# Kernel optimization log

Hardware: AMD Instinct MI355X
Metric: run time of the kernel (lower is better)

Reference implementation:

```python
import jax, jax.numpy as jnp
import numpy as np

NUM_CLASSES = 5
DIM = 512
NUM_HEADS = 8
B, N = 8, 256


def setup_inputs() -> dict:
    key = jax.random.key(0)
    ks = jax.random.split(key, 7)
    s = 1.0 / np.sqrt(DIM)
    return {
        "x": jax.random.normal(ks[0], (B, N, DIM), dtype=jnp.float32),
        "anchors": jax.random.normal(ks[1], (NUM_CLASSES, N, DIM), dtype=jnp.float32),
        "weights": jax.random.uniform(ks[2], (B, NUM_HEADS, NUM_CLASSES), dtype=jnp.float32),
        "qk_w": jax.random.normal(ks[3], (DIM, DIM), dtype=jnp.float32) * s,
        "v_w": jax.random.normal(ks[4], (DIM, DIM), dtype=jnp.float32) * s,
        "proj_w": jax.random.normal(ks[5], (DIM, DIM), dtype=jnp.float32) * s,
        "proj_b": jnp.zeros((DIM,), dtype=jnp.float32),
    }


def reference(x, anchors, weights, qk_w, v_w, proj_w, proj_b):
    Bx, Nx, C = x.shape
    H = NUM_HEADS
    hd = C // H
    scale = hd ** (-0.5)

    # v: [B, H, N, hd]
    v = (x @ v_w.T).reshape(Bx, Nx, H, hd).transpose(0, 2, 1, 3)
    # q: [B, H, N, hd]; k: [cls, H, N, hd] (shared qk projection)
    q = (x @ qk_w.T).reshape(Bx, Nx, H, hd).transpose(0, 2, 1, 3)
    k = (anchors @ qk_w.T).reshape(NUM_CLASSES, Nx, H, hd).transpose(0, 2, 1, 3)

    # a0: [B, cls, H, N, N]
    a0 = jnp.einsum("bhnd,chmd->bchnm", q, k) * scale
    left = jax.nn.relu(-a0)                         # relu of negative branch
    right = jax.nn.relu(jnp.swapaxes(a0, -2, -1))   # relu of transposed positive branch
    # second large NxN matmul, then softmax over dim=-2 (columns)
    attn = jax.nn.softmax(left @ right, axis=-2)    # [B, cls, H, N, N]

    # class-weighted combine: weights [B, H, cls] -> tmp [B, H, N, N]
    tmp = jnp.einsum("bhc,bchnm->bhnm", weights, attn)

    # (tmp @ v): [B, H, N, hd]; torch reshapes directly to (B, N, C) without permute
    out = (tmp @ v).reshape(Bx, Nx, C)
    out = out @ proj_w.T + proj_b
    return (out, a0)
```

## Files before the change

kernel.cpp:

```cpp
#include <hip/hip_runtime.h>
#include <hip/hip_fp16.h>
#include <cstdint>

#define BB 8
#define NN 256
#define NC 5
#define NH 8
#define DIM 512
#define HD 64

typedef _Float16 half_t;
typedef _Float16 h8 __attribute__((ext_vector_type(8)));
typedef _Float16 h4 __attribute__((ext_vector_type(4)));
typedef float f4 __attribute__((ext_vector_type(4)));
typedef uint32_t u4v __attribute__((ext_vector_type(4)));

__device__ __forceinline__ f4 mfma16(h8 a, h8 b, f4 c) {
  return __builtin_amdgcn_mfma_f32_16x16x32_f16(a, b, c, 0, 0, 0);
}

static __device__ const h8 HZERO = {(_Float16)0, (_Float16)0, (_Float16)0, (_Float16)0,
                                    (_Float16)0, (_Float16)0, (_Float16)0, (_Float16)0};

__device__ __forceinline__ h8 relu_pos_h8(h8 x) {
#if __has_builtin(__builtin_elementwise_max)
  return __builtin_elementwise_max(x, HZERO);
#else
  u4v u = __builtin_bit_cast(u4v, x);
  const u4v k1 = {0x00010001u, 0x00010001u, 0x00010001u, 0x00010001u};
  u4v s = (u >> 15) & k1;
  u4v m = (s << 16) - s;
  u = u & ~m;
  return __builtin_bit_cast(h8, u);
#endif
}

__device__ __forceinline__ h8 relu_neg_h8(h8 x) {
#if __has_builtin(__builtin_elementwise_max)
  return __builtin_elementwise_max(-x, HZERO);
#else
  u4v u = __builtin_bit_cast(u4v, x);
  const u4v k1 = {0x00010001u, 0x00010001u, 0x00010001u, 0x00010001u};
  const u4v ks = {0x80008000u, 0x80008000u, 0x80008000u, 0x80008000u};
  u4v s = (u >> 15) & k1;
  u4v m = (s << 16) - s;
  u = (u ^ ks) & m;
  return __builtin_bit_cast(h8, u);
#endif
}

__device__ __forceinline__ void barrier_lds() {
  __builtin_amdgcn_sched_barrier(0);
  asm volatile("s_waitcnt lgkmcnt(0)" ::: "memory");
  __builtin_amdgcn_s_barrier();
  asm volatile("" ::: "memory");
  __builtin_amdgcn_sched_barrier(0);
}

__global__ __launch_bounds__(256) void cvt_all(const float* __restrict__ x,
                                               const float* __restrict__ anchors,
                                               const float* __restrict__ qk_w,
                                               const float* __restrict__ v_w,
                                               const float* __restrict__ proj_w,
                                               half_t* __restrict__ x_h,
                                               half_t* __restrict__ anc_h,
                                               half_t* __restrict__ qk_h,
                                               half_t* __restrict__ v_wh,
                                               half_t* __restrict__ pw_h) {
  int i = blockIdx.x * 256 + threadIdx.x;
  const float* src;
  half_t* dst;
  int off;
  if (i < 262144)      { src = x;       dst = x_h;   off = i; }
  else if (i < 425984) { src = anchors; dst = anc_h; off = i - 262144; }
  else if (i < 491520) { src = qk_w;    dst = qk_h;  off = i - 425984; }
  else if (i < 557056) { src = v_w;     dst = v_wh;  off = i - 491520; }
  else                 { src = proj_w;  dst = pw_h;  off = i - 557056; }
  float4 v = ((const float4*)src)[off];
  h4 o;
  o[0] = (_Float16)v.x; o[1] = (_Float16)v.y; o[2] = (_Float16)v.z; o[3] = (_Float16)v.w;
  ((h4*)dst)[off] = o;
}

__global__ __launch_bounds__(256) void proj_all(const half_t* __restrict__ x_h,
                                                const half_t* __restrict__ anc_h,
                                                const half_t* __restrict__ qk_h,
                                                const half_t* __restrict__ v_wh,
                                                half_t* __restrict__ q_h,
                                                half_t* __restrict__ k_h,
                                                half_t* __restrict__ vT) {
  const int bx = blockIdx.x, by = blockIdx.y;
  const int tid = threadIdx.x;
  const int w = tid >> 6, lane = tid & 63;
  const int lr = lane & 15, lk = (lane >> 4) * 8, lg = lane >> 4;

  const half_t* A;
  const half_t* W;
  int mode, rt0;
  if (bx < 32)      { A = x_h;   W = qk_h; mode = 0; rt0 = bx * 64; }
  else if (bx < 52) { A = anc_h; W = qk_h; mode = 1; rt0 = (bx - 32) * 64; }
  else              { A = x_h;   W = v_wh; mode = 2; rt0 = (bx - 52) * 64; }

  const int row0 = rt0 + w * 16;
  const int col0 = by * 64;
  const f4 fz = {0.f, 0.f, 0.f, 0.f};
  f4 acc[4] = {fz, fz, fz, fz};
  const half_t* arow = A + (size_t)(row0 + lr) * DIM;

  if (mode != 2) {
    for (int k0 = 0; k0 < DIM; k0 += 32) {
      h8 a = *(const h8*)(arow + k0 + lk);
#pragma unroll
      for (int ct = 0; ct < 4; ++ct) {
        h8 b = *(const h8*)(W + (size_t)(col0 + ct * 16 + lr) * DIM + k0 + lk);
        acc[ct] = mfma16(a, b, acc[ct]);
      }
    }
    half_t* out = (mode == 0) ? q_h : k_h;
#pragma unroll
    for (int ct = 0; ct < 4; ++ct) {
      int col = col0 + ct * 16 + lr;
#pragma unroll
      for (int r = 0; r < 4; ++r) {
        int row = row0 + lg * 4 + r;
        out[(size_t)row * DIM + col] = (half_t)acc[ct][r];
      }
    }
  } else {
    for (int k0 = 0; k0 < DIM; k0 += 32) {
      h8 a = *(const h8*)(arow + k0 + lk);
#pragma unroll
      for (int ct = 0; ct < 4; ++ct) {
        h8 b = *(const h8*)(W + (size_t)(col0 + ct * 16 + lr) * DIM + k0 + lk);
        acc[ct] = mfma16(b, a, acc[ct]);
      }
    }
    const int xrow = row0 + lr;
#pragma unroll
    for (int ct = 0; ct < 4; ++ct) {
#pragma unroll
      for (int r = 0; r < 4; ++r) {
        int col = col0 + ct * 16 + lg * 4 + r;
        vT[(size_t)col * (BB * NN) + xrow] = (half_t)acc[ct][r];
      }
    }
  }
}

__global__ __launch_bounds__(1024, 4) void fused_attn8(const half_t* __restrict__ q_h,
                                                       const half_t* __restrict__ k_h,
                                                       const half_t* __restrict__ vT,
                                                       const float* __restrict__ weights,
                                                       float* __restrict__ a0_base,
                                                       half_t* __restrict__ U4) {
  extern __shared__ char smem[];
  half_t* a0s = (half_t*)smem;
  half_t* kst = (half_t*)(smem + 98304);
  half_t* vst = (half_t*)smem;
  half_t* pbuf = (half_t*)(smem + 32768);
  float2* scr = (float2*)(smem + 131072);
  float2* scr2 = (float2*)(smem + 147456);

  const int id = blockIdx.x;
  const int b = id / 40;
  const int rem = id % 40;
  const int c = rem / 8;
  const int h = rem & 7;

  const int tid = threadIdx.x;
  const int w = tid >> 6, lane = tid & 63;
  const int lr = lane & 15, lk = (lane >> 4) * 8, lg = lane >> 4;
  const int n0 = w * 16;
  const int sg = w & 7, cg = w >> 3;

  const half_t* qb = q_h + (size_t)(b * NN) * DIM + h * HD;
  const half_t* kb = k_h + (size_t)(c * NN) * DIM + h * HD;
  const half_t* vTb = vT + (size_t)(h * HD) * (BB * NN) + b * NN;
  float* a0out = a0_base + (size_t)((b * NC + c) * NH + h) * (NN * NN);
  const float wgt = weights[(b * NH + h) * NC + c];

  const f4 fz = {0.f, 0.f, 0.f, 0.f};

  h8 qf0 = *(const h8*)(qb + (size_t)(n0 + lr) * DIM + lk);
  h8 qf1 = *(const h8*)(qb + (size_t)(n0 + lr) * DIM + 32 + lk);

#pragma unroll
  for (int pass = 0; pass < 2; ++pass) {
    int slot = pass * 1024 + tid;
    int row = slot >> 3, k8 = (slot & 7) * 8;
    h8 val = *(const h8*)(kb + (size_t)row * DIM + k8);
    *(h8*)(kst + ((row * 64 + k8) ^ ((row & 7) << 3))) = val;
  }
  barrier_lds();

  f4 acc[16];
#pragma unroll
  for (int mt = 0; mt < 16; ++mt) {
    const int krow = mt * 16 + lr;
    h8 kf0 = *(const h8*)(kst + ((krow * 64 + lk) ^ ((krow & 7) << 3)));
    h8 kf1 = *(const h8*)(kst + ((krow * 64 + 32 + lk) ^ ((krow & 7) << 3)));
    acc[mt] = mfma16(kf0, qf0, fz);
    acc[mt] = mfma16(kf1, qf1, acc[mt]);
#pragma unroll
    for (int r = 0; r < 4; ++r) acc[mt][r] *= 0.125f;
  }
  barrier_lds();

  const int na = n0 + lr;
#pragma unroll
  for (int mt = 0; mt < 16; ++mt) {
    const int mb = mt * 16 + lg * 4;
    h4 hv;
#pragma unroll
    for (int r = 0; r < 4; ++r) hv[r] = (_Float16)acc[mt][r];
    *(h4*)(a0s + ((na * NN + mb) ^ ((na & 7) << 3))) = hv;
    *(f4*)(a0out + (size_t)na * NN + mb) = acc[mt];
  }
  barrier_lds();

  f4 sacc[8][2];
#pragma unroll
  for (int ct = 0; ct < 8; ++ct) {
    sacc[ct][0] = fz;
    sacc[ct][1] = fz;
  }
#pragma unroll
  for (int kc = 0; kc < 8; ++kc) {
    const int rl0 = sg * 32 + lr, rl1 = sg * 32 + 16 + lr;
    h8 La0 = relu_neg_h8(*(const h8*)(a0s + ((rl0 * NN + kc * 32 + lk) ^ ((rl0 & 7) << 3))));
    h8 La1 = relu_neg_h8(*(const h8*)(a0s + ((rl1 * NN + kc * 32 + lk) ^ ((rl1 & 7) << 3))));
#pragma unroll
    for (int ct = 0; ct < 8; ++ct) {
      const int rr = cg * 128 + ct * 16 + lr;
      h8 R = relu_pos_h8(*(const h8*)(a0s + ((rr * NN + kc * 32 + lk) ^ ((rr & 7) << 3))));
      sacc[ct][0] = mfma16(La0, R, sacc[ct][0]);
      sacc[ct][1] = mfma16(La1, R, sacc[ct][1]);
    }
  }

  float mw[8];
#pragma unroll
  for (int ct = 0; ct < 8; ++ct) {
    float v = 0.f;
#pragma unroll
    for (int rt = 0; rt < 2; ++rt)
#pragma unroll
      for (int r = 0; r < 4; ++r) v = fmaxf(v, sacc[ct][rt][r]);
    v = fmaxf(v, __shfl_xor(v, 16, 64));
    v = fmaxf(v, __shfl_xor(v, 32, 64));
    mw[ct] = v;
    float s = 0.f;
#pragma unroll
    for (int rt = 0; rt < 2; ++rt)
#pragma unroll
      for (int r = 0; r < 4; ++r) {
        float e = __expf(sacc[ct][rt][r] - v);
        sacc[ct][rt][r] = e;
        s += e;
      }
    s += __shfl_xor(s, 16, 64);
    s += __shfl_xor(s, 32, 64);
    if (lane < 16) {
      float2 t;
      t.x = v;
      t.y = s;
      scr[sg * 256 + cg * 128 + ct * 16 + lr] = t;
    }
  }
  barrier_lds();

  if (tid < 256) {
    float gm = 0.f;
#pragma unroll
    for (int ww = 0; ww < 8; ++ww) gm = fmaxf(gm, scr[ww * 256 + tid].x);
    float sg2 = 0.f;
#pragma unroll
    for (int ww = 0; ww < 8; ++ww) {
      float2 t = scr[ww * 256 + tid];
      sg2 += t.y * __expf(t.x - gm);
    }
    float2 r;
    r.x = gm;
    r.y = sg2;
    scr2[tid] = r;
  }
#pragma unroll
  for (int pass = 0; pass < 2; ++pass) {
    int slot = pass * 1024 + tid;
    int d = slot >> 5, m8 = (slot & 31) * 8;
    h8 vv = *(const h8*)(vTb + (size_t)d * (BB * NN) + m8);
    *(h8*)(vst + ((d * NN + m8) ^ ((d & 7) << 3))) = vv;
  }
  barrier_lds();

#pragma unroll
  for (int ct = 0; ct < 8; ++ct) {
    float2 t = scr2[cg * 128 + ct * 16 + lr];
    float fac = __expf(mw[ct] - t.x) * wgt / t.y;
#pragma unroll
    for (int rt = 0; rt < 2; ++rt)
#pragma unroll
      for (int r = 0; r < 4; ++r) sacc[ct][rt][r] *= fac;
  }

  half_t* pbw = pbuf + w * 1344;
  f4 uacc[4][2];
#pragma unroll
  for (int dt = 0; dt < 4; ++dt) {
    uacc[dt][0] = fz;
    uacc[dt][1] = fz;
  }
#pragma unroll
  for (int p = 0; p < 4; ++p) {
#pragma unroll
    for (int ctl = 0; ctl < 2; ++ctl) {
      const int ct = p * 2 + ctl;
#pragma unroll
      for (int rt = 0; rt < 2; ++rt) {
        h4 hv;
#pragma unroll
        for (int r = 0; r < 4; ++r) hv[r] = (_Float16)sacc[ct][rt][r];
        *(h4*)(pbw + (ctl * 16 + lr) * 42 + rt * 16 + lg * 4) = hv;
      }
    }
    h8 pf0, pf1;
#pragma unroll
    for (int e = 0; e < 8; ++e) {
      pf0[e] = pbw[(lg * 8 + e) * 42 + lr];
      pf1[e] = pbw[(lg * 8 + e) * 42 + 16 + lr];
    }
#pragma unroll
    for (int dt = 0; dt < 4; ++dt) {
      const int dr = dt * 16 + lr;
      h8 vf = *(const h8*)(vst + ((dr * NN + cg * 128 + p * 32 + lg * 8) ^ ((dr & 7) << 3)));
      uacc[dt][0] = mfma16(vf, pf0, uacc[dt][0]);
      uacc[dt][1] = mfma16(vf, pf1, uacc[dt][1]);
    }
  }

  half_t* U4b = U4 + (size_t)(((b * NC + c) * NH + h) * 2 + cg) * (NN * HD);
#pragma unroll
  for (int dt = 0; dt < 4; ++dt)
#pragma unroll
    for (int nt = 0; nt < 2; ++nt) {
      int n = sg * 32 + nt * 16 + lr;
      h4 hv;
#pragma unroll
      for (int r = 0; r < 4; ++r) hv[r] = (_Float16)uacc[dt][nt][r];
      *(h4*)(U4b + (size_t)n * HD + dt * 16 + lg * 4) = hv;
    }
}

__global__ __launch_bounds__(256) void reduce_u(const half_t* __restrict__ U4,
                                                half_t* __restrict__ out_head) {
  int t = blockIdx.x * 256 + threadIdx.x;
  int bh = t >> 11;
  int e = (t & 2047) * 8;
  int b = bh >> 3, h = bh & 7;
  float acc[8] = {0.f, 0.f, 0.f, 0.f, 0.f, 0.f, 0.f, 0.f};
#pragma unroll
  for (int c = 0; c < NC; ++c)
#pragma unroll
    for (int qq = 0; qq < 2; ++qq) {
      h8 u = *(const h8*)(U4 + (size_t)(((b * NC + c) * NH + h) * 2 + qq) * (NN * HD) + e);
#pragma unroll
      for (int j = 0; j < 8; ++j) acc[j] += (float)u[j];
    }
  h8 o;
#pragma unroll
  for (int j = 0; j < 8; ++j) o[j] = (_Float16)acc[j];
  *(h8*)(out_head + (size_t)bh * (NN * HD) + e) = o;
}

__global__ __launch_bounds__(256) void out_proj(const half_t* __restrict__ out_head,
                                                const half_t* __restrict__ pw_h,
                                                const float* __restrict__ pb,
                                                float* __restrict__ out0) {
  const int tid = threadIdx.x;
  const int w = tid >> 6, lane = tid & 63;
  const int lr = lane & 15, lk = (lane >> 4) * 8, lg = lane >> 4;
  const int row0 = blockIdx.x * 64 + w * 16;
  const int col0 = blockIdx.y * 64;
  const int r_ = row0 + lr;
  const int b = r_ >> 8, i = r_ & 255;
  const int hh = i >> 5;
  const f4 fz = {0.f, 0.f, 0.f, 0.f};
  f4 acc[4] = {fz, fz, fz, fz};
  for (int k0 = 0; k0 < DIM; k0 += 32) {
    const int k = k0 + lk;
    const int n = ((i & 31) << 3) | (k >> 6);
    const int d = k & 63;
    h8 a = *(const h8*)(out_head + (size_t)((b * NH + hh) * NN + n) * HD + d);
#pragma unroll
    for (int ct = 0; ct < 4; ++ct) {
      h8 bf = *(const h8*)(pw_h + (size_t)(col0 + ct * 16 + lr) * DIM + k0 + lk);
      acc[ct] = mfma16(a, bf, acc[ct]);
    }
  }
#pragma unroll
  for (int ct = 0; ct < 4; ++ct) {
    int col = col0 + ct * 16 + lr;
    float bias = pb[col];
#pragma unroll
    for (int r = 0; r < 4; ++r) {
      int row = row0 + lg * 4 + r;
      out0[(size_t)row * DIM + col] = acc[ct][r] + bias;
    }
  }
}

extern "C" void kernel_launch(void* const* d_in, const int* in_sizes, int n_in,
                              void* d_out, int out_size, void* d_ws, size_t ws_size,
                              hipStream_t stream) {
  const float* x = (const float*)d_in[0];
  const float* anchors = (const float*)d_in[1];
  const float* weights = (const float*)d_in[2];
  const float* qk_w = (const float*)d_in[3];
  const float* v_w = (const float*)d_in[4];
  const float* proj_w = (const float*)d_in[5];
  const float* proj_b = (const float*)d_in[6];

  float* out0 = (float*)d_out;
  float* a0_out = out0 + (size_t)BB * NN * DIM;

  char* ws = (char*)d_ws;
  const size_t MB = 1024 * 1024;
  half_t* x_h   = (half_t*)(ws);
  half_t* anc_h = (half_t*)(ws + 2 * MB);
  half_t* qk_h  = (half_t*)(ws + 3407872);
  half_t* v_wh  = (half_t*)(ws + 3932160);
  half_t* U4    = (half_t*)(ws);
  half_t* pw_h     = (half_t*)(ws + 20 * MB);
  half_t* q_h      = (half_t*)(ws + 20 * MB + 524288);
  half_t* k_h      = (half_t*)(ws + 22 * MB + 524288);
  half_t* vT       = (half_t*)(ws + 24 * MB);
  half_t* out_head = (half_t*)(ws + 26 * MB);

  cvt_all<<<dim3(2432), 256, 0, stream>>>(x, anchors, qk_w, v_w, proj_w,
                                          x_h, anc_h, qk_h, v_wh, pw_h);

  proj_all<<<dim3(84, 8), 256, 0, stream>>>(x_h, anc_h, qk_h, v_wh, q_h, k_h, vT);

  const size_t lds_bytes = 131072 + 16384 + 2048;
  fused_attn8<<<dim3(BB * NC * NH), 1024, lds_bytes, stream>>>(q_h, k_h, vT, weights,
                                                               a0_out, U4);

  reduce_u<<<dim3(512), 256, 0, stream>>>(U4, out_head);

  out_proj<<<dim3(32, 8), 256, 0, stream>>>(out_head, pw_h, proj_b, out0);

  (void)in_sizes; (void)n_in; (void)out_size; (void)ws_size;
}
```

Measured before the change: 126.5 us.

## Split a0 GEMM into its own kernel and fuse class reduction into output projection

The q·k score GEMM moves out of the large fused attention kernel into a separate 4x-wider grid kernel that writes fp32 a0. The attention kernel then reloads a0 from global memory, converts it to fp16 in LDS, and reads V directly from global memory instead of staging it in LDS. The class/half reduction of U4 is folded into a new output-projection kernel that stages the reduced rows in LDS, which removes one launch. The aim is more parallelism for the score GEMM and fewer launches, at the cost of re-reading the 84MB a0 tensor and uncached global V loads inside the MFMA loop.

Result: slower. 165.0 us (+30.4%).

```diff
diff --git a/kernel.cpp b/kernel.cpp
--- a/kernel.cpp
+++ b/kernel.cpp
@@ -147,16 +147,58 @@
   }
 }
 
-__global__ __launch_bounds__(1024, 4) void fused_attn8(const half_t* __restrict__ q_h,
-                                                       const half_t* __restrict__ k_h,
-                                                       const half_t* __restrict__ vT,
-                                                       const float* __restrict__ weights,
-                                                       float* __restrict__ a0_base,
-                                                       half_t* __restrict__ U4) {
+__global__ __launch_bounds__(256, 4) void a0_gemm(const half_t* __restrict__ q_h,
+                                                  const half_t* __restrict__ k_h,
+                                                  float* __restrict__ a0_base) {
+  __shared__ half_t kst[256 * 64];
+  const int bid = blockIdx.x;
+  const int task = bid >> 2, quarter = bid & 3;
+  const int b = task / 40;
+  const int rem = task % 40;
+  const int c = rem / 8;
+  const int h = rem & 7;
+
+  const int tid = threadIdx.x;
+  const int w = tid >> 6, lane = tid & 63;
+  const int lr = lane & 15, lk = (lane >> 4) * 8, lg = lane >> 4;
+
+  const half_t* qb = q_h + (size_t)(b * NN) * DIM + h * HD;
+  const half_t* kb = k_h + (size_t)(c * NN) * DIM + h * HD;
+  float* a0out = a0_base + (size_t)((b * NC + c) * NH + h) * (NN * NN);
+
+#pragma unroll
+  for (int pass = 0; pass < 8; ++pass) {
+    int slot = pass * 256 + tid;
+    int row = slot >> 3, k8 = (slot & 7) * 8;
+    *(h8*)(kst + ((row * 64 + k8) ^ ((row & 7) << 3))) =
+        *(const h8*)(kb + (size_t)row * DIM + k8);
+  }
+  __syncthreads();
+
+  const int n0 = quarter * 64 + w * 16;
+  h8 qf0 = *(const h8*)(qb + (size_t)(n0 + lr) * DIM + lk);
+  h8 qf1 = *(const h8*)(qb + (size_t)(n0 + lr) * DIM + 32 + lk);
+  const f4 fz = {0.f, 0.f, 0.f, 0.f};
+  const int na = n0 + lr;
+#pragma unroll
+  for (int mt = 0; mt < 16; ++mt) {
+    const int krow = mt * 16 + lr;
+    h8 kf0 = *(const h8*)(kst + ((krow * 64 + lk) ^ ((krow & 7) << 3)));
+    h8 kf1 = *(const h8*)(kst + ((krow * 64 + 32 + lk) ^ ((krow & 7) << 3)));
+    f4 acc = mfma16(kf0, qf0, fz);
+    acc = mfma16(kf1, qf1, acc);
+#pragma unroll
+    for (int r = 0; r < 4; ++r) acc[r] *= 0.125f;
+    *(f4*)(a0out + (size_t)na * NN + mt * 16 + lg * 4) = acc;
+  }
+}
+
+__global__ __launch_bounds__(1024, 4) void attn_sm(const float* __restrict__ a0_base,
+                                                   const half_t* __restrict__ vT,
+                                                   const float* __restrict__ weights,
+                                                   half_t* __restrict__ U4) {
   extern __shared__ char smem[];
   half_t* a0s = (half_t*)smem;
-  half_t* kst = (half_t*)(smem + 98304);
-  half_t* vst = (half_t*)smem;
   half_t* pbuf = (half_t*)(smem + 32768);
   float2* scr = (float2*)(smem + 131072);
   float2* scr2 = (float2*)(smem + 147456);
@@ -170,51 +212,28 @@
   const int tid = threadIdx.x;
   const int w = tid >> 6, lane = tid & 63;
   const int lr = lane & 15, lk = (lane >> 4) * 8, lg = lane >> 4;
-  const int n0 = w * 16;
   const int sg = w & 7, cg = w >> 3;
 
-  const half_t* qb = q_h + (size_t)(b * NN) * DIM + h * HD;
-  const half_t* kb = k_h + (size_t)(c * NN) * DIM + h * HD;
+  const float* a0f = a0_base + (size_t)((b * NC + c) * NH + h) * (NN * NN);
   const half_t* vTb = vT + (size_t)(h * HD) * (BB * NN) + b * NN;
-  float* a0out = a0_base + (size_t)((b * NC + c) * NH + h) * (NN * NN);
   const float wgt = weights[(b * NH + h) * NC + c];
 
   const f4 fz = {0.f, 0.f, 0.f, 0.f};
 
-  h8 qf0 = *(const h8*)(qb + (size_t)(n0 + lr) * DIM + lk);
-  h8 qf1 = *(const h8*)(qb + (size_t)(n0 + lr) * DIM + 32 + lk);
-
-#pragma unroll
-  for (int pass = 0; pass < 2; ++pass) {
+#pragma unroll
+  for (int pass = 0; pass < 8; ++pass) {
     int slot = pass * 1024 + tid;
-    int row = slot >> 3, k8 = (slot & 7) * 8;
-    h8 val = *(const h8*)(kb + (size_t)row * DIM + k8);
-    *(h8*)(kst + ((row * 64 + k8) ^ ((row & 7) << 3))) = val;
-  }
-  barrier_lds();
-
-  f4 acc[16];
-#pragma unroll
-  for (int mt = 0; mt < 16; ++mt) {
-    const int krow = mt * 16 + lr;
-    h8 kf0 = *(const h8*)(kst + ((krow * 64 + lk) ^ ((krow & 7) << 3)));
-    h8 kf1 = *(const h8*)(kst + ((krow * 64 + 32 + lk) ^ ((krow & 7) << 3)));
-    acc[mt] = mfma16(kf0, qf0, fz);
-    acc[mt] = mfma16(kf1, qf1, acc[mt]);
-#pragma unroll
-    for (int r = 0; r < 4; ++r) acc[mt][r] *= 0.125f;
-  }
-  barrier_lds();
-
-  const int na = n0 + lr;
-#pragma unroll
-  for (int mt = 0; mt < 16; ++mt) {
-    const int mb = mt * 16 + lg * 4;
-    h4 hv;
-#pragma unroll
-    for (int r = 0; r < 4; ++r) hv[r] = (_Float16)acc[mt][r];
-    *(h4*)(a0s + ((na * NN + mb) ^ ((na & 7) << 3))) = hv;
-    *(f4*)(a0out + (size_t)na * NN + mb) = acc[mt];
+    int n = slot >> 5, m8 = (slot & 31) * 8;
+    const float* p = a0f + (size_t)n * NN + m8;
+    f4 va = *(const f4*)p;
+    f4 vb = *(const f4*)(p + 4);
+    h8 hv;
+#pragma unroll
+    for (int r = 0; r < 4; ++r) {
+      hv[r] = (_Float16)va[r];
+      hv[4 + r] = (_Float16)vb[r];
+    }
+    *(h8*)(a0s + ((n * NN + m8) ^ ((n & 7) << 3))) = hv;
   }
   barrier_lds();
 
@@ -284,13 +303,6 @@
     r.y = sg2;
     scr2[tid] = r;
   }
-#pragma unroll
-  for (int pass = 0; pass < 2; ++pass) {
-    int slot = pass * 1024 + tid;
-    int d = slot >> 5, m8 = (slot & 31) * 8;
-    h8 vv = *(const h8*)(vTb + (size_t)d * (BB * NN) + m8);
-    *(h8*)(vst + ((d * NN + m8) ^ ((d & 7) << 3))) = vv;
-  }
   barrier_lds();
 
 #pragma unroll
@@ -331,8 +343,7 @@
     }
 #pragma unroll
     for (int dt = 0; dt < 4; ++dt) {
-      const int dr = dt * 16 + lr;
-      h8 vf = *(const h8*)(vst + ((dr * NN + cg * 128 + p * 32 + lg * 8) ^ ((dr & 7) << 3)));
+      h8 vf = *(const h8*)(vTb + (size_t)(dt * 16 + lr) * (BB * NN) + cg * 128 + p * 32 + lg * 8);
       uacc[dt][0] = mfma16(vf, pf0, uacc[dt][0]);
       uacc[dt][1] = mfma16(vf, pf1, uacc[dt][1]);
     }
@@ -351,61 +362,71 @@
     }
 }
 
-__global__ __launch_bounds__(256) void reduce_u(const half_t* __restrict__ U4,
-                                                half_t* __restrict__ out_head) {
-  int t = blockIdx.x * 256 + threadIdx.x;
-  int bh = t >> 11;
-  int e = (t & 2047) * 8;
-  int b = bh >> 3, h = bh & 7;
-  float acc[8] = {0.f, 0.f, 0.f, 0.f, 0.f, 0.f, 0.f, 0.f};
-#pragma unroll
-  for (int c = 0; c < NC; ++c)
-#pragma unroll
-    for (int qq = 0; qq < 2; ++qq) {
-      h8 u = *(const h8*)(U4 + (size_t)(((b * NC + c) * NH + h) * 2 + qq) * (NN * HD) + e);
-#pragma unroll
-      for (int j = 0; j < 8; ++j) acc[j] += (float)u[j];
-    }
-  h8 o;
-#pragma unroll
-  for (int j = 0; j < 8; ++j) o[j] = (_Float16)acc[j];
-  *(h8*)(out_head + (size_t)bh * (NN * HD) + e) = o;
-}
-
-__global__ __launch_bounds__(256) void out_proj(const half_t* __restrict__ out_head,
-                                                const half_t* __restrict__ pw_h,
-                                                const float* __restrict__ pb,
-                                                float* __restrict__ out0) {
+__global__ __launch_bounds__(256) void out_projA(const half_t* __restrict__ U4,
+                                                 const half_t* __restrict__ pw_h,
+                                                 const float* __restrict__ pb,
+                                                 float* __restrict__ out0) {
+  __shared__ half_t Ast[32 * 520];
+  const int bid = blockIdx.x;
+  const int b = bid >> 3, hh = bid & 7;
   const int tid = threadIdx.x;
+
+  {
+    const int il = tid >> 3, kk = tid & 7;
+    const int n = (il << 3) | kk;
+    const half_t* base = U4 + ((size_t)(b * NC * NH + hh) * 2) * (NN * HD) + (size_t)n * HD;
+#pragma unroll
+    for (int d0 = 0; d0 < HD; d0 += 8) {
+      float a8[8] = {0.f, 0.f, 0.f, 0.f, 0.f, 0.f, 0.f, 0.f};
+#pragma unroll
+      for (int cc = 0; cc < NC; ++cc)
+#pragma unroll
+        for (int qq = 0; qq < 2; ++qq) {
+          h8 u = *(const h8*)(base + (size_t)(cc * NH * 2 + qq) * (NN * HD) + d0);
+#pragma unroll
+          for (int j = 0; j < 8; ++j) a8[j] += (float)u[j];
+        }
+      h8 o;
+#pragma unroll
+      for (int j = 0; j < 8; ++j) o[j] = (_Float16)a8[j];
+      *(h8*)(&Ast[il * 520 + kk * 64 + d0]) = o;
+    }
+  }
+  __syncthreads();
+
   const int w = tid >> 6, lane = tid & 63;
   const int lr = lane & 15, lk = (lane >> 4) * 8, lg = lane >> 4;
-  const int row0 = blockIdx.x * 64 + w * 16;
-  const int col0 = blockIdx.y * 64;
-  const int r_ = row0 + lr;
-  const int b = r_ >> 8, i = r_ & 255;
-  const int hh = i >> 5;
+  const int col0 = w * 128;
   const f4 fz = {0.f, 0.f, 0.f, 0.f};
-  f4 acc[4] = {fz, fz, fz, fz};
-  for (int k0 = 0; k0 < DIM; k0 += 32) {
-    const int k = k0 + lk;
-    const int n = ((i & 31) << 3) | (k >> 6);
-    const int d = k & 63;
-    h8 a = *(const h8*)(out_head + (size_t)((b * NH + hh) * NN + n) * HD + d);
-#pragma unroll
-    for (int ct = 0; ct < 4; ++ct) {
-      h8 bf = *(const h8*)(pw_h + (size_t)(col0 + ct * 16 + lr) * DIM + k0 + lk);
-      acc[ct] = mfma16(a, bf, acc[ct]);
-    }
-  }
-#pragma unroll
-  for (int ct = 0; ct < 4; ++ct) {
+  f4 acc[2][8];
+#pragma unroll
+  for (int rt = 0; rt < 2; ++rt)
+#pragma unroll
+    for (int ct = 0; ct < 8; ++ct) acc[rt][ct] = fz;
+
+  for (int kc = 0; kc < 16; ++kc) {
+    h8 a0f = *(const h8*)(&Ast[(lr)*520 + kc * 32 + lk]);
+    h8 a1f = *(const h8*)(&Ast[(16 + lr) * 520 + kc * 32 + lk]);
+#pragma unroll
+    for (int ct = 0; ct < 8; ++ct) {
+      h8 bf = *(const h8*)(pw_h + (size_t)(col0 + ct * 16 + lr) * DIM + kc * 32 + lk);
+      acc[0][ct] = mfma16(a0f, bf, acc[0][ct]);
+      acc[1][ct] = mfma16(a1f, bf, acc[1][ct]);
+    }
+  }
+
+  const int row_base = b * NN + hh * 32;
+#pragma unroll
+  for (int ct = 0; ct < 8; ++ct) {
     int col = col0 + ct * 16 + lr;
     float bias = pb[col];
 #pragma unroll
-    for (int r = 0; r < 4; ++r) {
-      int row = row0 + lg * 4 + r;
-      out0[(size_t)row * DIM + col] = acc[ct][r] + bias;
-    }
+    for (int rt = 0; rt < 2; ++rt)
+#pragma unroll
+      for (int r = 0; r < 4; ++r) {
+        int row = row_base + rt * 16 + lg * 4 + r;
+        out0[(size_t)row * DIM + col] = acc[rt][ct][r] + bias;
+      }
   }
 }
 
@@ -430,24 +451,22 @@
   half_t* qk_h  = (half_t*)(ws + 3407872);
   half_t* v_wh  = (half_t*)(ws + 3932160);
   half_t* U4    = (half_t*)(ws);
-  half_t* pw_h     = (half_t*)(ws + 20 * MB);
-  half_t* q_h      = (half_t*)(ws + 20 * MB + 524288);
-  half_t* k_h      = (half_t*)(ws + 22 * MB + 524288);
-  half_t* vT       = (half_t*)(ws + 24 * MB);
-  half_t* out_head = (half_t*)(ws + 26 * MB);
+  half_t* pw_h = (half_t*)(ws + 20 * MB);
+  half_t* q_h  = (half_t*)(ws + 20 * MB + 524288);
+  half_t* k_h  = (half_t*)(ws + 22 * MB + 524288);
+  half_t* vT   = (half_t*)(ws + 24 * MB);
 
   cvt_all<<<dim3(2432), 256, 0, stream>>>(x, anchors, qk_w, v_w, proj_w,
                                           x_h, anc_h, qk_h, v_wh, pw_h);
 
   proj_all<<<dim3(84, 8), 256, 0, stream>>>(x_h, anc_h, qk_h, v_wh, q_h, k_h, vT);
 
+  a0_gemm<<<dim3(BB * NC * NH * 4), 256, 0, stream>>>(q_h, k_h, a0_out);
+
   const size_t lds_bytes = 131072 + 16384 + 2048;
-  fused_attn8<<<dim3(BB * NC * NH), 1024, lds_bytes, stream>>>(q_h, k_h, vT, weights,
-                                                               a0_out, U4);
-
-  reduce_u<<<dim3(512), 256, 0, stream>>>(U4, out_head);
-
-  out_proj<<<dim3(32, 8), 256, 0, stream>>>(out_head, pw_h, proj_b, out0);
+  attn_sm<<<dim3(BB * NC * NH), 1024, lds_bytes, stream>>>(a0_out, vT, weights, U4);
+
+  out_projA<<<dim3(64), 256, 0, stream>>>(U4, pw_h, proj_b, out0);
 
   (void)in_sizes; (void)n_in; (void)out_size; (void)ws_size;
 }
```
